# Optimization experiments

Hardware: AMD Instinct MI355X
Metric: run time of the kernel (lower is better)

Reference implementation:

```python
import jax, jax.numpy as jnp
import numpy as np
from jax import lax

# Model dims (match init_kwargs / input_specs)
B, T, N_IN, N_MID, N_OUT = 256, 100, 784, 1024, 10
L_TAU = 0.8  # state decay


def setup_inputs() -> dict:
    key = jax.random.key(0)
    ks = jax.random.split(key, 10)
    x = jax.random.uniform(ks[0], (B, T, N_IN), dtype=jnp.float32)  # input spikes/rates
    y = jax.random.randint(ks[1], (B,), 0, N_OUT, dtype=jnp.int64)

    def lin(k, fan_in, fan_out):
        return jax.random.normal(k, (fan_in, fan_out), dtype=jnp.float32) / np.sqrt(fan_in)

    return {
        "x": x, "y": y,
        "W1": lin(ks[2], N_IN, N_MID),  "b1": jnp.zeros((N_MID,), jnp.float32),
        "W2": lin(ks[3], N_MID, N_MID), "b2": jnp.zeros((N_MID,), jnp.float32),
        "W3": lin(ks[4], N_MID, N_MID), "b3": jnp.zeros((N_MID,), jnp.float32),
        "W4": lin(ks[5], N_MID, N_OUT), "b4": jnp.zeros((N_OUT,), jnp.float32),
    }


def _snu(s, y_prev, x_in, W, b):
    # SNU cell (soft): s_t = relu(W x_t + tau * s_{t-1} * (1 - y_{t-1})); y_t = sigmoid(s_t + b)
    s = jax.nn.relu(x_in @ W + L_TAU * s * (1.0 - y_prev))
    y_out = jax.nn.sigmoid(s + b)
    return s, y_out


def reference(x, y, W1, b1, W2, b2, W3, b3, W4, b4):
    bsz = x.shape[0]
    zeros = lambda n: jnp.zeros((bsz, n), x.dtype)
    carry0 = (zeros(N_MID), zeros(N_MID), zeros(N_MID), zeros(N_MID),
              zeros(N_MID), zeros(N_MID), zeros(N_OUT), zeros(N_OUT))

    def step(carry, x_t):
        s1, y1, s2, y2, s3, y3, s4, y4 = carry
        s1, y1 = _snu(s1, y1, x_t, W1, b1)
        s2, y2 = _snu(s2, y2, y1, W2, b2)
        s3, y3 = _snu(s3, y3, y2, W3, b3)
        s4, y4 = _snu(s4, y4, y3, W4, b4)
        return (s1, y1, s2, y2, s3, y3, s4, y4), y4

    xs = jnp.transpose(x, (1, 0, 2))  # [T, B, n_in]
    _, outs = lax.scan(step, carry0, xs)  # outs: [T, B, n_out]
    # out_rec also stacked the initial zero output; it contributes 0 to the sum
    m = jnp.sum(outs, axis=0)  # [B, n_out]
    logp = jax.nn.log_softmax(m, axis=-1)
    loss = -jnp.mean(jnp.take_along_axis(logp, y[:, None], axis=1))
    return loss, m
```

## Files before the change

kernel.cpp:

```cpp
#include <hip/hip_runtime.h>
#include <hip/hip_bf16.h>


#define BDIM 256
#define TT   100
#define TP   112
#define BB   256
#define MM2  (BB * TP)
#define NMID 1024
#define K1   784
#define K1P  896
#define NOUT 10
#define N4P  16
#define L_TAU 0.8f

#define NBLK 256
#define ZST  102

typedef __attribute__((ext_vector_type(4))) int   int4x;
typedef __attribute__((ext_vector_type(8))) int   int8x;
typedef __attribute__((ext_vector_type(4))) float f32x4;

__device__ __forceinline__ void async_copy16(const void* g, void* l) {
    __builtin_amdgcn_global_load_lds(
        (const __attribute__((address_space(1))) unsigned int*)g,
        (__attribute__((address_space(3))) unsigned int*)l,
        16, 0, 0);
}

__device__ __forceinline__ unsigned short f2bf(float f) {
    __hip_bfloat16 h = __float2bfloat16(f);
    return __builtin_bit_cast(unsigned short, h);
}
__device__ __forceinline__ float bf2f(unsigned short u) {
    return __uint_as_float((unsigned)u << 16);
}

__global__ void convert_x(const float* __restrict__ X, unsigned char* __restrict__ XB) {
    int m = blockIdx.x;
    int b = m & (BB - 1);
    int t = m >> 8;
    int th = threadIdx.x;
    if (th >= K1P / 4) return;
    int pk = 0;
    if (th < K1 / 4) {
        float4 v = *(const float4*)(X + ((long)b * TT + t) * K1 + th * 4);
        pk = __builtin_amdgcn_cvt_pk_fp8_f32(v.x, v.y, 0, false);
        pk = __builtin_amdgcn_cvt_pk_fp8_f32(v.z, v.w, pk, true);
    }
    *(int*)(XB + ((long)b * TP + t) * K1P + th * 4) = pk;
}

__device__ __forceinline__ void tc_body(const float* __restrict__ W,
                                        unsigned char* __restrict__ WT,
                                        int K, int N, int Kpad,
                                        int bx, int by, int tidx) {
    __shared__ float tile[32][33];
    int k0 = bx * 32;
    int n0 = by * 32;
    int tx = tidx & 31, ty = tidx >> 5;
    #pragma unroll
    for (int i = 0; i < 4; ++i) {
        int k = k0 + ty + i * 8;
        tile[ty + i * 8][tx] = (k < K) ? W[(long)k * N + n0 + tx] : 0.0f;
    }
    __syncthreads();
    int nl = tidx >> 3, kq = tidx & 7;
    int pk = __builtin_amdgcn_cvt_pk_fp8_f32(tile[kq * 4 + 0][nl], tile[kq * 4 + 1][nl], 0, false);
    pk     = __builtin_amdgcn_cvt_pk_fp8_f32(tile[kq * 4 + 2][nl], tile[kq * 4 + 3][nl], pk, true);
    *(int*)(WT + (long)(n0 + nl) * Kpad + k0 + kq * 4) = pk;
}

__global__ void transpose_convert(const float* __restrict__ W, unsigned char* __restrict__ WT,
                                  int K, int N, int Kpad) {
    tc_body(W, WT, K, N, Kpad, blockIdx.x, blockIdx.y, threadIdx.x);
}

__global__ void transpose_convert2(const float* __restrict__ Wa, unsigned char* __restrict__ Ta,
                                   const float* __restrict__ Wb, unsigned char* __restrict__ Tb) {
    const float* W = blockIdx.z ? Wb : Wa;
    unsigned char* T = blockIdx.z ? Tb : Ta;
    tc_body(W, T, NMID, NMID, NMID, blockIdx.x, blockIdx.y, threadIdx.x);
}

__global__ void convert_w4(const float* __restrict__ W4, unsigned char* __restrict__ W4T) {
    int tid = blockIdx.x * BDIM + threadIdx.x;
    int n = tid >> 8;
    int k4 = (tid & 255) * 4;
    float v0 = 0, v1 = 0, v2 = 0, v3 = 0;
    if (n < NOUT) {
        v0 = W4[(k4 + 0) * NOUT + n];
        v1 = W4[(k4 + 1) * NOUT + n];
        v2 = W4[(k4 + 2) * NOUT + n];
        v3 = W4[(k4 + 3) * NOUT + n];
    }
    int pk = __builtin_amdgcn_cvt_pk_fp8_f32(v0, v1, 0, false);
    pk     = __builtin_amdgcn_cvt_pk_fp8_f32(v2, v3, pk, true);
    *(int*)(W4T + (long)n * NMID + k4) = pk;
}

__device__ __forceinline__ void stage_tile(const unsigned char* Aptr,
                                           const unsigned char* Bptr,
                                           unsigned char* As, unsigned char* Bs,
                                           int srow, int lch, int Kp, int k0) {
    #pragma unroll
    for (int i = 0; i < 4; ++i)
        if (srow + i * 32 < TP)
            async_copy16(Aptr + (long)(i * 32) * Kp + k0,
                         &As[(srow + i * 32) * 128 + lch * 16]);
    #pragma unroll
    for (int i = 0; i < 8; ++i)
        async_copy16(Bptr + (long)(i * 32) * Kp + k0,
                     &Bs[(srow + i * 32) * 128 + lch * 16]);
}

__global__ __launch_bounds__(256, 3) void gemm_snu_fused(
    const unsigned char* __restrict__ A,
    const unsigned char* __restrict__ BT,
    const float* __restrict__ bias,
    unsigned char* __restrict__ Y,
    int Kp)
{
    __shared__ unsigned char smem[52224];
    unsigned char* As = smem;
    unsigned char* Bs = smem + 14336;
    unsigned short* Zs = (unsigned short*)smem;

    const int tid  = threadIdx.x;
    const int wave = tid >> 6;
    const int lane = tid & 63;

    const int l   = blockIdx.x;
    const int xcd = l & 7;
    const int p   = l >> 3;
    const int b   = xcd * 32 + (p >> 2);
    const int bn  = (p & 3) * NBLK;

    const long arow0 = (long)b * TP;

    f32x4 acc[7][4] = {};

    const int srow = tid >> 3;
    const int lch  = tid & 7;
    const int gch  = lch ^ (srow & 7);
    const unsigned char* Aptr = A  + (arow0 + srow) * Kp + gch * 16;
    const unsigned char* Bptr = BT + (long)(bn + srow) * Kp + gch * 16;

    const int mrow = lane & 15;
    const int g    = lane >> 4;
    const int wc   = wave * 64;

    for (int k0 = 0; k0 < Kp; k0 += 128) {
        stage_tile(Aptr, Bptr, As, Bs, srow, lch, Kp, k0);
        __syncthreads();

        int8x bfr[4];
        #pragma unroll
        for (int j = 0; j < 4; ++j) {
            int row = wc + j * 16 + mrow;
            int r7  = row & 7;
            int4x lo = *(const int4x*)&Bs[row * 128 + ((2 * g    ) ^ r7) * 16];
            int4x hi = *(const int4x*)&Bs[row * 128 + ((2 * g + 1) ^ r7) * 16];
            bfr[j][0] = lo[0]; bfr[j][1] = lo[1]; bfr[j][2] = lo[2]; bfr[j][3] = lo[3];
            bfr[j][4] = hi[0]; bfr[j][5] = hi[1]; bfr[j][6] = hi[2]; bfr[j][7] = hi[3];
        }
        #pragma unroll
        for (int i = 0; i < 7; ++i) {
            int row = i * 16 + mrow;
            int r7  = row & 7;
            int4x lo = *(const int4x*)&As[row * 128 + ((2 * g    ) ^ r7) * 16];
            int4x hi = *(const int4x*)&As[row * 128 + ((2 * g + 1) ^ r7) * 16];
            int8x af;
            af[0] = lo[0]; af[1] = lo[1]; af[2] = lo[2]; af[3] = lo[3];
            af[4] = hi[0]; af[5] = hi[1]; af[6] = hi[2]; af[7] = hi[3];
            #pragma unroll
            for (int j = 0; j < 4; ++j)
                acc[i][j] = __builtin_amdgcn_mfma_scale_f32_16x16x128_f8f6f4(
                    bfr[j], af, acc[i][j],
                    0, 0,
                    0, 0x7F,
                    0, 0x7F);
        }
        __syncthreads();
    }

    #pragma unroll
    for (int i = 0; i < 7; ++i)
        #pragma unroll
        for (int j = 0; j < 4; ++j) {
            int t  = i * 16 + mrow;
            int nn = wc + j * 16 + g * 4;
            if (t < TT)
                #pragma unroll
                for (int r = 0; r < 4; ++r)
                    Zs[(nn + r) * ZST + t] = f2bf(acc[i][j][r]);
        }
    __syncthreads();

    {
        int n = tid;
        float bv = bias[bn + n];
        float s = 0.0f, u = 1.0f;
        const unsigned short* zp = Zs + n * ZST;
        unsigned char* yp = Y + arow0 * NMID + bn + n;
        for (int t = 0; t < TT; ++t) {
            float z = bf2f(zp[t]);
            s = fmaxf(fmaf(L_TAU * s, u, z), 0.0f);
            float e = __expf(s + bv);
            u = __builtin_amdgcn_rcpf(1.0f + e);
            float yv = 1.0f - u;
            int pk = __builtin_amdgcn_cvt_pk_fp8_f32(yv, yv, 0, false);
            yp[(long)t * NMID] = (unsigned char)(pk & 0xFF);
        }
    }
}

__global__ __launch_bounds__(256) void layer4_gemm(const unsigned char* __restrict__ Y3,
                                                   const unsigned char* __restrict__ W4T,
                                                   float* __restrict__ Z4) {
    const int tid  = threadIdx.x;
    const int wave = tid >> 6;
    const int lane = tid & 63;
    const int mrow = lane & 15;
    const int g    = lane >> 4;
    const int row  = blockIdx.x * 64 + wave * 16 + mrow;
    const unsigned char* ap = Y3  + (long)row  * NMID + g * 32;
    const unsigned char* wp = W4T + (long)mrow * NMID + g * 32;
    f32x4 acc = {};
    #pragma unroll
    for (int kt = 0; kt < 8; ++kt) {
        int4x alo = *(const int4x*)(ap + kt * 128);
        int4x ahi = *(const int4x*)(ap + kt * 128 + 16);
        int4x wlo = *(const int4x*)(wp + kt * 128);
        int4x whi = *(const int4x*)(wp + kt * 128 + 16);
        int8x af, bf;
        af[0] = alo[0]; af[1] = alo[1]; af[2] = alo[2]; af[3] = alo[3];
        af[4] = ahi[0]; af[5] = ahi[1]; af[6] = ahi[2]; af[7] = ahi[3];
        bf[0] = wlo[0]; bf[1] = wlo[1]; bf[2] = wlo[2]; bf[3] = wlo[3];
        bf[4] = whi[0]; bf[5] = whi[1]; bf[6] = whi[2]; bf[7] = whi[3];
        acc = __builtin_amdgcn_mfma_scale_f32_16x16x128_f8f6f4(
            bf, af, acc, 0, 0, 0, 0x7F, 0, 0x7F);
    }
    *(f32x4*)&Z4[(long)row * N4P + g * 4] = acc;
}

__global__ void snu4_recur(const float* __restrict__ Z4, const float* __restrict__ b4,
                           float* __restrict__ m_out) {
    int idx = blockIdx.x * BDIM + threadIdx.x;
    int n = idx & 15;
    int b = idx >> 4;
    if (n >= NOUT) return;
    float bv = b4[n];
    float s = 0.0f, u = 1.0f, msum = 0.0f;
    const float* zp = Z4 + (long)b * TP * N4P + n;
    for (int t0 = 0; t0 < TT; t0 += 4) {
        float z[4];
        #pragma unroll
        for (int j = 0; j < 4; ++j)
            z[j] = zp[(t0 + j) * N4P];
        #pragma unroll
        for (int j = 0; j < 4; ++j) {
            s = fmaxf(fmaf(L_TAU * s, u, z[j]), 0.0f);
            float e = __expf(s + bv);
            u = __builtin_amdgcn_rcpf(1.0f + e);
            msum += 1.0f - u;
        }
    }
    m_out[b * NOUT + n] = msum;
}

__global__ void loss_kernel(const float* __restrict__ m, const int* __restrict__ y,
                            float* __restrict__ out) {
    __shared__ float red[BDIM];
    int b = threadIdx.x;
    float v[NOUT];
    float mx = -1e30f;
    #pragma unroll
    for (int n = 0; n < NOUT; ++n) { v[n] = m[b * NOUT + n]; mx = fmaxf(mx, v[n]); }
    float se = 0.0f;
    #pragma unroll
    for (int n = 0; n < NOUT; ++n) se += __expf(v[n] - mx);
    float lse = mx + __logf(se);
    int lbl = y[b];
    float vy = 0.0f;
    #pragma unroll
    for (int n = 0; n < NOUT; ++n) if (n == lbl) vy = v[n];
    red[b] = -(vy - lse);
    __syncthreads();
    for (int off = 128; off; off >>= 1) {
        if (b < off) red[b] += red[b + off];
        __syncthreads();
    }
    if (b == 0) out[0] = red[0] / (float)BB;
}

extern "C" void kernel_launch(void* const* d_in, const int* in_sizes, int n_in,
                              void* d_out, int out_size, void* d_ws, size_t ws_size,
                              hipStream_t stream) {
    const float* x  = (const float*)d_in[0];
    const int*   y  = (const int*)  d_in[1];
    const float* W1 = (const float*)d_in[2];
    const float* b1 = (const float*)d_in[3];
    const float* W2 = (const float*)d_in[4];
    const float* b2 = (const float*)d_in[5];
    const float* W3 = (const float*)d_in[6];
    const float* b3 = (const float*)d_in[7];
    const float* W4 = (const float*)d_in[8];
    const float* b4 = (const float*)d_in[9];
    float* out = (float*)d_out;

    char* ws = (char*)d_ws;
    size_t off = 0;
    auto alloc = [&](size_t bytes) {
        char* p = ws + off;
        off = (off + bytes + 255) & ~(size_t)255;
        return (void*)p;
    };
    unsigned char* XB  = (unsigned char*)alloc((size_t)MM2 * K1P);
    unsigned char* W1T = (unsigned char*)alloc((size_t)NMID * K1P);
    unsigned char* W2T = (unsigned char*)alloc((size_t)NMID * NMID);
    unsigned char* W3T = (unsigned char*)alloc((size_t)NMID * NMID);
    unsigned char* W4T = (unsigned char*)alloc((size_t)N4P * NMID);
    unsigned char* Ya  = (unsigned char*)alloc((size_t)MM2 * NMID);
    unsigned char* Yb  = (unsigned char*)alloc((size_t)MM2 * NMID);
    float*         Z4  = (float*)        alloc((size_t)MM2 * N4P * 4);

    convert_x<<<BB * TT, BDIM, 0, stream>>>(x, XB);
    transpose_convert<<<dim3(K1P / 32, NMID / 32), BDIM, 0, stream>>>(W1, W1T, K1, NMID, K1P);
    transpose_convert2<<<dim3(NMID / 32, NMID / 32, 2), BDIM, 0, stream>>>(W2, W2T, W3, W3T);
    convert_w4<<<N4P * NMID / 4 / BDIM, BDIM, 0, stream>>>(W4, W4T);

    const int fblocks = BB * (NMID / NBLK);
    gemm_snu_fused<<<fblocks, BDIM, 0, stream>>>(XB, W1T, b1, Ya, K1P);
    gemm_snu_fused<<<fblocks, BDIM, 0, stream>>>(Ya, W2T, b2, Yb, NMID);
    gemm_snu_fused<<<fblocks, BDIM, 0, stream>>>(Yb, W3T, b3, Ya, NMID);
    layer4_gemm<<<MM2 / 64, BDIM, 0, stream>>>(Ya, W4T, Z4);
    snu4_recur<<<(BB * N4P) / BDIM, BDIM, 0, stream>>>(Z4, b4, out + 1);
    loss_kernel<<<1, BDIM, 0, stream>>>(out + 1, y, out);
}
```

Before: 336.7 us.

## Double-buffer fused GEMM tiles with split-phase async staging and barriers

Replaces the single-buffered K loop, which waited on a full barrier every tile, with two LDS buffers. The next tile's A and lower-half B are prefetched while the current tile is computed, and the upper-half B is loaded during the second compute phase, using explicit vmcnt waits and s_setprio around the MFMA blocks. Each wave now covers 32 columns from each B half rather than 64 contiguous ones. The LDS footprint grows to 96KB and launch bounds drop to one block per CU, so latency hiding now depends on the pipeline instead of occupancy.

```diff
diff --git a/kernel.cpp b/kernel.cpp
--- a/kernel.cpp
+++ b/kernel.cpp
@@ -16,6 +16,7 @@
 
 #define NBLK 256
 #define ZST  102
+#define BUFSZ 49152
 
 typedef __attribute__((ext_vector_type(4))) int   int4x;
 typedef __attribute__((ext_vector_type(8))) int   int8x;
@@ -99,31 +100,14 @@
     *(int*)(W4T + (long)n * NMID + k4) = pk;
 }
 
-__device__ __forceinline__ void stage_tile(const unsigned char* Aptr,
-                                           const unsigned char* Bptr,
-                                           unsigned char* As, unsigned char* Bs,
-                                           int srow, int lch, int Kp, int k0) {
-    #pragma unroll
-    for (int i = 0; i < 4; ++i)
-        if (srow + i * 32 < TP)
-            async_copy16(Aptr + (long)(i * 32) * Kp + k0,
-                         &As[(srow + i * 32) * 128 + lch * 16]);
-    #pragma unroll
-    for (int i = 0; i < 8; ++i)
-        async_copy16(Bptr + (long)(i * 32) * Kp + k0,
-                     &Bs[(srow + i * 32) * 128 + lch * 16]);
-}
-
-__global__ __launch_bounds__(256, 3) void gemm_snu_fused(
+__global__ __launch_bounds__(256, 1) void gemm_snu_fused(
     const unsigned char* __restrict__ A,
     const unsigned char* __restrict__ BT,
     const float* __restrict__ bias,
     unsigned char* __restrict__ Y,
     int Kp)
 {
-    __shared__ unsigned char smem[52224];
-    unsigned char* As = smem;
-    unsigned char* Bs = smem + 14336;
+    __shared__ unsigned char smem[2 * BUFSZ];
     unsigned short* Zs = (unsigned short*)smem;
 
     const int tid  = threadIdx.x;
@@ -148,19 +132,58 @@
 
     const int mrow = lane & 15;
     const int g    = lane >> 4;
-    const int wc   = wave * 64;
-
-    for (int k0 = 0; k0 < Kp; k0 += 128) {
-        stage_tile(Aptr, Bptr, As, Bs, srow, lch, Kp, k0);
-        __syncthreads();
-
-        int8x bfr[4];
-        #pragma unroll
-        for (int j = 0; j < 4; ++j) {
+    const int wc   = wave * 32;
+
+    const int NT = Kp >> 7;
+
+    auto stage_h1 = [&](unsigned char* buf, int k0) {
+        unsigned char* As = buf;
+        unsigned char* Bl = buf + 16384;
+        #pragma unroll
+        for (int i = 0; i < 4; ++i)
+            async_copy16(Aptr + (long)(i * 32) * Kp + k0,
+                         &As[(srow + i * 32) * 128 + lch * 16]);
+        #pragma unroll
+        for (int i = 0; i < 4; ++i)
+            async_copy16(Bptr + (long)(i * 32) * Kp + k0,
+                         &Bl[(srow + i * 32) * 128 + lch * 16]);
+    };
+    auto stage_h2 = [&](unsigned char* buf, int k0) {
+        unsigned char* Bh = buf + 32768;
+        #pragma unroll
+        for (int i = 0; i < 4; ++i)
+            async_copy16(Bptr + (long)(128 + i * 32) * Kp + k0,
+                         &Bh[(srow + i * 32) * 128 + lch * 16]);
+    };
+
+    stage_h1(smem, 0);
+    stage_h2(smem, 0);
+
+    int8x af[7];
+    for (int t = 0; t < NT; ++t) {
+        unsigned char* cbuf = smem + (t & 1) * BUFSZ;
+        unsigned char* nbuf = smem + ((t & 1) ^ 1) * BUFSZ;
+        const unsigned char* As = cbuf;
+        const unsigned char* Bl = cbuf + 16384;
+        const unsigned char* Bh = cbuf + 32768;
+        const int k0n = (t + 1) << 7;
+
+        if (t + 1 < NT) {
+            stage_h1(nbuf, k0n);
+            asm volatile("s_waitcnt vmcnt(12)" ::: "memory");
+        } else {
+            asm volatile("s_waitcnt vmcnt(4)" ::: "memory");
+        }
+        __builtin_amdgcn_s_barrier();
+        asm volatile("" ::: "memory");
+
+        int8x bfr[2];
+        #pragma unroll
+        for (int j = 0; j < 2; ++j) {
             int row = wc + j * 16 + mrow;
             int r7  = row & 7;
-            int4x lo = *(const int4x*)&Bs[row * 128 + ((2 * g    ) ^ r7) * 16];
-            int4x hi = *(const int4x*)&Bs[row * 128 + ((2 * g + 1) ^ r7) * 16];
+            int4x lo = *(const int4x*)&Bl[row * 128 + ((2 * g    ) ^ r7) * 16];
+            int4x hi = *(const int4x*)&Bl[row * 128 + ((2 * g + 1) ^ r7) * 16];
             bfr[j][0] = lo[0]; bfr[j][1] = lo[1]; bfr[j][2] = lo[2]; bfr[j][3] = lo[3];
             bfr[j][4] = hi[0]; bfr[j][5] = hi[1]; bfr[j][6] = hi[2]; bfr[j][7] = hi[3];
         }
@@ -170,30 +193,61 @@
             int r7  = row & 7;
             int4x lo = *(const int4x*)&As[row * 128 + ((2 * g    ) ^ r7) * 16];
             int4x hi = *(const int4x*)&As[row * 128 + ((2 * g + 1) ^ r7) * 16];
-            int8x af;
-            af[0] = lo[0]; af[1] = lo[1]; af[2] = lo[2]; af[3] = lo[3];
-            af[4] = hi[0]; af[5] = hi[1]; af[6] = hi[2]; af[7] = hi[3];
+            af[i][0] = lo[0]; af[i][1] = lo[1]; af[i][2] = lo[2]; af[i][3] = lo[3];
+            af[i][4] = hi[0]; af[i][5] = hi[1]; af[i][6] = hi[2]; af[i][7] = hi[3];
+        }
+        __builtin_amdgcn_s_setprio(1);
+        #pragma unroll
+        for (int i = 0; i < 7; ++i)
             #pragma unroll
-            for (int j = 0; j < 4; ++j)
+            for (int j = 0; j < 2; ++j)
                 acc[i][j] = __builtin_amdgcn_mfma_scale_f32_16x16x128_f8f6f4(
-                    bfr[j], af, acc[i][j],
+                    bfr[j], af[i], acc[i][j],
                     0, 0,
                     0, 0x7F,
                     0, 0x7F);
-        }
-        __syncthreads();
-    }
+        __builtin_amdgcn_s_setprio(0);
+
+        if (t + 1 < NT) {
+            stage_h2(nbuf, k0n);
+            asm volatile("s_waitcnt vmcnt(12)" ::: "memory");
+        } else {
+            asm volatile("s_waitcnt vmcnt(0)" ::: "memory");
+        }
+        __builtin_amdgcn_s_barrier();
+        asm volatile("" ::: "memory");
+
+        #pragma unroll
+        for (int j = 0; j < 2; ++j) {
+            int row = wc + j * 16 + mrow;
+            int r7  = row & 7;
+            int4x lo = *(const int4x*)&Bh[row * 128 + ((2 * g    ) ^ r7) * 16];
+            int4x hi = *(const int4x*)&Bh[row * 128 + ((2 * g + 1) ^ r7) * 16];
+            bfr[j][0] = lo[0]; bfr[j][1] = lo[1]; bfr[j][2] = lo[2]; bfr[j][3] = lo[3];
+            bfr[j][4] = hi[0]; bfr[j][5] = hi[1]; bfr[j][6] = hi[2]; bfr[j][7] = hi[3];
+        }
+        __builtin_amdgcn_s_setprio(1);
+        #pragma unroll
+        for (int i = 0; i < 7; ++i)
+            #pragma unroll
+            for (int j = 0; j < 2; ++j)
+                acc[i][2 + j] = __builtin_amdgcn_mfma_scale_f32_16x16x128_f8f6f4(
+                    bfr[j], af[i], acc[i][2 + j],
+                    0, 0, 0, 0x7F, 0, 0x7F);
+        __builtin_amdgcn_s_setprio(0);
+    }
+    __syncthreads();
 
     #pragma unroll
     for (int i = 0; i < 7; ++i)
         #pragma unroll
-        for (int j = 0; j < 4; ++j) {
+        for (int jj = 0; jj < 4; ++jj) {
             int t  = i * 16 + mrow;
-            int nn = wc + j * 16 + g * 4;
+            int nn = (jj < 2 ? wc + jj * 16 : 128 + wc + (jj - 2) * 16) + g * 4;
             if (t < TT)
                 #pragma unroll
                 for (int r = 0; r < 4; ++r)
-                    Zs[(nn + r) * ZST + t] = f2bf(acc[i][j][r]);
+                    Zs[(nn + r) * ZST + t] = f2bf(acc[i][jj][r]);
         }
     __syncthreads();
 
```

Result: slower. 349.2 us (+3.7%).
